# Kernel tuning notes

Measured on AMD Instinct MI355X. Metric: run time of the kernel, lower is better.

Reference implementation:

```python
import jax, jax.numpy as jnp
import numpy as np

DIM = 512
NUM_HEADS = 8
HEAD_DIM = DIM // NUM_HEADS
GAMMA = 1.0


def setup_inputs() -> dict:
    key = jax.random.key(0)
    ks = jax.random.split(key, 10)
    B, S = 2, 2048
    x_real = jax.random.normal(ks[0], (B, S, DIM), dtype=jnp.float32)
    x_imag = jax.random.normal(ks[1], (B, S, DIM), dtype=jnp.float32)
    def xavier(k, fan_in, fan_out):
        lim = float(np.sqrt(6.0 / (fan_in + fan_out)))
        return jax.random.uniform(k, (fan_in, fan_out), jnp.float32, -lim, lim)
    # torch Linear(in,out): weight [out,in]; we store transposed [in,out]
    Wq = xavier(ks[2], 2 * DIM, DIM); bq = jnp.zeros((DIM,), jnp.float32)
    Wk = xavier(ks[3], 2 * DIM, DIM); bk = jnp.zeros((DIM,), jnp.float32)
    Wv = xavier(ks[4], 2 * DIM, DIM); bv = jnp.zeros((DIM,), jnp.float32)
    Wo = xavier(ks[5], DIM, 2 * DIM); bo = jnp.zeros((2 * DIM,), jnp.float32)
    return {"x_real": x_real, "x_imag": x_imag, "Wq": Wq, "bq": bq,
            "Wk": Wk, "bk": bk, "Wv": Wv, "bv": bv, "Wo": Wo, "bo": bo}


def reference(x_real, x_imag, Wq, bq, Wk, bk, Wv, bv, Wo, bo):
    B, S, _ = x_real.shape
    real_embed = jnp.concatenate([x_real, x_imag], axis=-1)  # [B,S,2*dim]
    def proj(W, b):
        y = real_embed @ W + b                               # [B,S,dim]
        return y.reshape(B, S, NUM_HEADS, HEAD_DIM).transpose(0, 2, 1, 3)  # [B,H,S,d]
    Q = proj(Wq, bq)
    K = proj(Wk, bk)
    V = proj(Wv, bv)
    # softmax over head_dim is broadcast-invariant, so the Bhattacharyya
    # coefficient sum_d sqrt(p_i[d]*q_j[d]) factorizes into a matmul.
    sp = jnp.sqrt(jax.nn.softmax(Q, axis=-1))  # [B,H,S,d]
    sq = jnp.sqrt(jax.nn.softmax(K, axis=-1))  # [B,H,S,d]
    bc = jnp.einsum('bhid,bhjd->bhij', sp, sq)  # Bhattacharyya coeff [B,H,S,S]
    bc = jnp.clip(bc, -1.0, 1.0)
    dist = jnp.arccos(bc)
    attn = jax.nn.softmax(-GAMMA * dist * dist, axis=-1)  # [B,H,S,S]
    attended = jnp.einsum('bhij,bhjd->bhid', attn, V)
    attended = attended.transpose(0, 2, 1, 3).reshape(B, S, DIM)
    out = attended @ Wo + bo  # [B,S,2*dim] = concat(real_out, imag_out)
    return out
```

## Files before the change

### kernel.cpp

```cpp
#include <hip/hip_runtime.h>
#include <math.h>


typedef __attribute__((ext_vector_type(8))) short short8;
typedef __attribute__((ext_vector_type(4))) short bf16x4;
typedef __attribute__((ext_vector_type(4))) float f32x4;
typedef __attribute__((ext_vector_type(2))) float f32x2;

#define MFMA(a, b, c) __builtin_amdgcn_mfma_f32_16x16x32_bf16((a), (b), (c), 0, 0, 0)

static __device__ __forceinline__ short f2bf(float f) {
    unsigned u = __float_as_uint(f);
    u += 0x7fffu + ((u >> 16) & 1u);
    return (short)(u >> 16);
}

static __device__ __forceinline__ void gld_lds16(const short* g, short* l) {
    __builtin_amdgcn_global_load_lds(
        (const __attribute__((address_space(1))) unsigned int*)g,
        (__attribute__((address_space(3))) unsigned int*)l, 16, 0, 0);
}

__global__ __launch_bounds__(256) void convert_x(
    const float* __restrict__ xr, const float* __restrict__ xi,
    short* __restrict__ xb)
{
    int idx = blockIdx.x * 256 + threadIdx.x;
    int e = idx << 2;
    int m = e >> 10, k = e & 1023;
    const float* src = (k < 512) ? xr : xi;
    float4 t = *(const float4*)(src + (size_t)m * 512 + (k & 511));
    unsigned lo = (unsigned short)f2bf(t.x) | ((unsigned)(unsigned short)f2bf(t.y) << 16);
    unsigned hi = (unsigned short)f2bf(t.z) | ((unsigned)(unsigned short)f2bf(t.w) << 16);
    uint2 o; o.x = lo; o.y = hi;
    *(uint2*)(xb + e) = o;
}

__global__ __launch_bounds__(256) void transpose_w(
    const float* __restrict__ Wq, const float* __restrict__ Wk,
    const float* __restrict__ Wv, const float* __restrict__ Wo,
    short* __restrict__ wqt, short* __restrict__ wkt,
    short* __restrict__ wvt, short* __restrict__ wot)
{
    __shared__ float t[32][33];
    const int z = blockIdx.z;
    const float* src = (z == 0) ? Wq : (z == 1) ? Wk : (z == 2) ? Wv : Wo;
    short* dst = (z == 0) ? wqt : (z == 1) ? wkt : (z == 2) ? wvt : wot;
    const int K = (z < 3) ? 1024 : 512;
    const int N = (z < 3) ? 512 : 1024;
    const int n0 = blockIdx.x << 5, k0 = blockIdx.y << 5;
    if (n0 >= N || k0 >= K) return;
    const int tx = threadIdx.x & 31, ty = threadIdx.x >> 5;
    #pragma unroll
    for (int i = 0; i < 4; ++i)
        t[ty + 8 * i][tx] = src[(size_t)(k0 + ty + 8 * i) * N + n0 + tx];
    __syncthreads();
    #pragma unroll
    for (int i = 0; i < 4; ++i)
        dst[(size_t)(n0 + ty + 8 * i) * K + k0 + tx] = f2bf(t[tx][ty + 8 * i]);
}

__global__ __launch_bounds__(128, 4) void qkv_mfma(
    const short* __restrict__ xb, const short* __restrict__ wcat,
    const float* __restrict__ bq, const float* __restrict__ bk,
    const float* __restrict__ bv,
    short* __restrict__ sp, short* __restrict__ sq, short* __restrict__ vt)
{
    __shared__ short As[3][128 * 32];
    __shared__ short Bs[3][64 * 32];
    const int jb = blockIdx.x;
    const int m0 = blockIdx.y << 7;
    const int tid = threadIdx.x;
    const int w = tid >> 6, lane = tid & 63;
    const int l = lane & 15, quad = lane >> 4;

    const int srow = lane >> 2;
    const int sseg = (lane & 3) << 3;
    const short* gA = xb   + (size_t)(m0        + (w << 6) + srow) * 1024 + sseg;
    const short* gB = wcat + (size_t)((jb << 6) + (w << 5) + srow) * 1024 + sseg;

    auto STAGE = [&](int bb, int kk) {
        const int k0 = kk << 5;
        #pragma unroll
        for (int t = 0; t < 4; ++t)
            gld_lds16(gA + k0 + t * 16 * 1024, &As[bb][((w << 2) + t) << 9]);
        #pragma unroll
        for (int t = 0; t < 2; ++t)
            gld_lds16(gB + k0 + t * 16 * 1024, &Bs[bb][((w << 1) + t) << 9]);
    };

    STAGE(0, 0);
    STAGE(1, 1);
    asm volatile("s_waitcnt vmcnt(6)" ::: "memory");
    __builtin_amdgcn_s_barrier();

    const f32x4 z4 = {0.f, 0.f, 0.f, 0.f};
    f32x4 acc[4][4];
    #pragma unroll
    for (int i = 0; i < 4; ++i)
        #pragma unroll
        for (int j = 0; j < 4; ++j) acc[i][j] = z4;

    int cb = 0, sb = 2;
    #pragma unroll 1
    for (int kt = 0; kt < 32; ++kt) {
        STAGE(sb, (kt + 2) & 31);
        const short* Al = &As[cb][(w << 6) << 5];
        const short* Bl = &Bs[cb][0];
        short8 af[4], bfr[4];
        #pragma unroll
        for (int i = 0; i < 4; ++i)
            af[i] = *(const short8*)(Al + (((i << 4) + l) << 5) + (quad << 3));
        #pragma unroll
        for (int j = 0; j < 4; ++j)
            bfr[j] = *(const short8*)(Bl + (((j << 4) + l) << 5) + (quad << 3));
        #pragma unroll
        for (int i = 0; i < 4; ++i)
            #pragma unroll
            for (int j = 0; j < 4; ++j)
                acc[i][j] = MFMA(af[i], bfr[j], acc[i][j]);
        asm volatile("s_waitcnt vmcnt(6)" ::: "memory");
        __builtin_amdgcn_s_barrier();
        cb = (cb == 2) ? 0 : cb + 1;
        sb = (sb == 2) ? 0 : sb + 1;
    }
    asm volatile("s_waitcnt vmcnt(0)" ::: "memory");

    const int op = jb >> 3;
    const int h  = jb & 7;

    if (op < 2) {
        short* dst = (op == 0) ? sp : sq;
        const float* bias = (op == 0) ? bq : bk;
        float bcol[4];
        #pragma unroll
        for (int nt = 0; nt < 4; ++nt) bcol[nt] = bias[(h << 6) + (nt << 4) + l];
        #pragma unroll
        for (int i = 0; i < 4; ++i) {
            #pragma unroll
            for (int reg = 0; reg < 4; ++reg) {
                const int r = m0 + (w << 6) + (i << 4) + (quad << 2) + reg;
                const int b = r >> 11, s = r & 2047;
                float v[4];
                #pragma unroll
                for (int nt = 0; nt < 4; ++nt) v[nt] = acc[i][nt][reg] + bcol[nt];
                float mx = fmaxf(fmaxf(v[0], v[1]), fmaxf(v[2], v[3]));
                #pragma unroll
                for (int msk = 1; msk < 16; msk <<= 1) mx = fmaxf(mx, __shfl_xor(mx, msk));
                float e[4], ssum = 0.f;
                #pragma unroll
                for (int nt = 0; nt < 4; ++nt) { e[nt] = __expf(v[nt] - mx); ssum += e[nt]; }
                #pragma unroll
                for (int msk = 1; msk < 16; msk <<= 1) ssum += __shfl_xor(ssum, msk);
                float inv = 1.0f / ssum;
                short* o = dst + ((size_t)((b << 3) + h) * 2048 + s) * 64 + l;
                #pragma unroll
                for (int nt = 0; nt < 4; ++nt)
                    o[nt << 4] = f2bf(sqrtf(e[nt] * inv));
            }
        }
    } else {
        float bcol[4];
        #pragma unroll
        for (int nt = 0; nt < 4; ++nt) bcol[nt] = bv[(h << 6) + (nt << 4) + l];
        #pragma unroll
        for (int i = 0; i < 4; ++i) {
            const int sb2 = m0 + (w << 6) + (i << 4) + (quad << 2);
            const int b = sb2 >> 11, s = sb2 & 2047;
            #pragma unroll
            for (int nt = 0; nt < 4; ++nt) {
                const int d = (nt << 4) + l;
                bf16x4 pk;
                #pragma unroll
                for (int reg = 0; reg < 4; ++reg)
                    pk[reg] = f2bf(acc[i][nt][reg] + bcol[nt]);
                *(bf16x4*)(vt + ((size_t)((b << 3) + h) * 64 + d) * 2048 + s) = pk;
            }
        }
    }
}

__global__ __launch_bounds__(256, 4) void attn_mfma(
    const short* __restrict__ sp, const short* __restrict__ sq,
    const short* __restrict__ vt, short* __restrict__ attB)
{
    __shared__ __align__(16) short sqT[2][64 * 64];
    __shared__ __align__(16) short vtT[2][64 * 64];
    __shared__ __align__(16) short Pb[4][16 * 64];
    __shared__ float denB[4][16];
    const int bh = blockIdx.y;
    const int m0 = blockIdx.x << 6;
    const int tid = threadIdx.x;
    const int w = tid >> 6, lane = tid & 63;
    const int l = lane & 15, quad = lane >> 4;
    const int l7 = l & 7;

    const short* spB = sp + (size_t)bh * 2048 * 64;
    const short* sqB = sq + (size_t)bh * 2048 * 64;
    const short* vtB = vt + (size_t)bh * 64 * 2048;

    const short* apr = spB + (size_t)(m0 + w * 16 + l) * 64 + quad * 8;
    short8 aq0 = *(const short8*)(apr);
    short8 aq1 = *(const short8*)(apr + 32);
    short8 nq0 = aq0 ^ (short)0x8000;
    short8 nq1 = aq1 ^ (short)0x8000;

    const int srow = tid >> 2;
    const int scol = (tid & 3) * 16;
    const short* sqG = sqB + (size_t)srow * 64 + scol;
    const short* vtG = vtB + (size_t)srow * 2048 + scol;
    const int sl0 = (tid & 3) << 1;
    const int sw0 = srow * 64 + (((sl0    ) ^ (srow & 7)) << 3);
    const int sw1 = srow * 64 + (((sl0 | 1) ^ (srow & 7)) << 3);

    const int sRd = (quad ^ l7) << 3;

    {
        short8 a0 = *(const short8*)(sqG);
        short8 a1 = *(const short8*)(sqG + 8);
        short8 b0 = *(const short8*)(vtG);
        short8 b1 = *(const short8*)(vtG + 8);
        *(short8*)(&sqT[0][sw0]) = a0;
        *(short8*)(&sqT[0][sw1]) = a1;
        *(short8*)(&vtT[0][sw0]) = b0;
        *(short8*)(&vtT[0][sw1]) = b1;
    }
    __syncthreads();

    const f32x4 z4 = {0.f, 0.f, 0.f, 0.f};
    const f32x4 ones4 = {1.f, 1.f, 1.f, 1.f};
    f32x4 acc[4] = {z4, z4, z4, z4};
    f32x2 den2 = {0.f, 0.f};
    short* Pw = &Pb[w][0];

    #pragma unroll 1
    for (int jt = 0; jt < 32; ++jt) {
        const int cb = jt & 1, nb = cb ^ 1;
        const int j0n = ((jt + 1) & 31) << 6;
        short8 na0 = *(const short8*)(sqG + (size_t)j0n * 64);
        short8 na1 = *(const short8*)(sqG + (size_t)j0n * 64 + 8);
        short8 nb0 = *(const short8*)(vtG + j0n);
        short8 nb1 = *(const short8*)(vtG + j0n + 8);

        const short* sqL = &sqT[cb][0];
        #pragma unroll
        for (int nt = 0; nt < 4; ++nt) {
            const short* ar = sqL + ((nt * 16 + l) << 6);
            short8 sa0 = *(const short8*)(ar + sRd);
            short8 sa1 = *(const short8*)(ar + (sRd ^ 32));
            f32x4 p = MFMA(sa0, nq0, ones4);
            p = MFMA(sa1, nq1, p);
            f32x2 u01 = {p[0], p[1]};
            f32x2 u23 = {p[2], p[3]};
            const f32x2 zz = {0.f, 0.f};
#if __has_builtin(__builtin_elementwise_max)
            u01 = __builtin_elementwise_max(u01, zz);
            u23 = __builtin_elementwise_max(u23, zz);
#else
            u01.x = fmaxf(u01.x, 0.f); u01.y = fmaxf(u01.y, 0.f);
            u23.x = fmaxf(u23.x, 0.f); u23.y = fmaxf(u23.y, 0.f);
#endif
            f32x2 t01 = {0.000922f, 0.000922f};
            f32x2 t23 = t01;
            t01 = t01 * u01 + 0.00152228f;  t23 = t23 * u23 + 0.00152228f;
            t01 = t01 * u01 + 0.00384801f;  t23 = t23 * u23 + 0.00384801f;
            t01 = t01 * u01 + 0.01015873f;  t23 = t23 * u23 + 0.01015873f;
            t01 = t01 * u01 + 0.02857143f;  t23 = t23 * u23 + 0.02857143f;
            t01 = t01 * u01 + 0.08888889f;  t23 = t23 * u23 + 0.08888889f;
            t01 = t01 * u01 + 0.33333333f;  t23 = t23 * u23 + 0.33333333f;
            t01 = t01 * u01 + 2.0f;         t23 = t23 * u23 + 2.0f;
            f32x2 w01 = u01 * t01;
            f32x2 w23 = u23 * t23;
            float e0 = __expf(-w01.x), e1 = __expf(-w01.y);
            float e2 = __expf(-w23.x), e3 = __expf(-w23.y);
            f32x2 es = {e0 + e2, e1 + e3};
            den2 += es;
            uint2 pk;
            pk.x = (__float_as_uint(e0) >> 16) | (__float_as_uint(e1) & 0xffff0000u);
            pk.y = (__float_as_uint(e2) >> 16) | (__float_as_uint(e3) & 0xffff0000u);
            *(uint2*)(&Pw[(l << 6) + ((((nt << 1) + (quad >> 1)) ^ l7) << 3)
                          + ((quad & 1) << 2)]) = pk;
        }

        const short* pr = Pw + (l << 6);
        short8 pa0 = *(const short8*)(pr + sRd);
        short8 pa1 = *(const short8*)(pr + (sRd ^ 32));
        const short* vL = &vtT[cb][0];
        #pragma unroll
        for (int t4 = 0; t4 < 4; ++t4) {
            const short* vr = vL + ((t4 * 16 + l) << 6);
            short8 vb0 = *(const short8*)(vr + sRd);
            short8 vb1 = *(const short8*)(vr + (sRd ^ 32));
            acc[t4] = MFMA(pa0, vb0, acc[t4]);
            acc[t4] = MFMA(pa1, vb1, acc[t4]);
        }

        *(short8*)(&sqT[nb][sw0]) = na0;
        *(short8*)(&sqT[nb][sw1]) = na1;
        *(short8*)(&vtT[nb][sw0]) = nb0;
        *(short8*)(&vtT[nb][sw1]) = nb1;
        __syncthreads();
    }

    float den = den2.x + den2.y;
    den += __shfl_xor(den, 16);
    den += __shfl_xor(den, 32);
    if (lane < 16) denB[w][l] = den;
    float invd[4];
    #pragma unroll
    for (int reg = 0; reg < 4; ++reg)
        invd[reg] = 1.0f / denB[w][quad * 4 + reg];

    const int b = bh >> 3, hh = bh & 7;
    #pragma unroll
    for (int t4 = 0; t4 < 4; ++t4)
        #pragma unroll
        for (int reg = 0; reg < 4; ++reg) {
            const int row = m0 + w * 16 + quad * 4 + reg;
            attB[((size_t)(b * 2048 + row)) * 512 + hh * 64 + t4 * 16 + l] =
                f2bf(acc[t4][reg] * invd[reg]);
        }
}

__global__ __launch_bounds__(256, 3) void out_mfma(
    const short* __restrict__ attB, const short* __restrict__ wot,
    const float* __restrict__ bo, float* __restrict__ out)
{
    __shared__ short As[3][128 * 32];
    __shared__ short Bs[3][64 * 32];
    const int nb0 = blockIdx.x << 6;
    const int m0 = blockIdx.y << 7;
    const int tid = threadIdx.x;
    const int w = tid >> 6, lane = tid & 63;
    const int l = lane & 15, quad = lane >> 4;

    const short* gA = attB + (size_t)(m0  + (w << 4) + (lane >> 2)) * 512 + ((lane & 3) << 3);
    const short* gB = wot  + (size_t)(nb0 + (w << 4) + (lane >> 2)) * 512 + ((lane & 3) << 3);

    auto STAGE = [&](int bb, int kk) {
        const int k0 = kk << 5;
        gld_lds16(gA + k0,            &As[bb][w << 9]);
        gld_lds16(gA + k0 + 64 * 512, &As[bb][(w + 4) << 9]);
        gld_lds16(gB + k0,            &Bs[bb][w << 9]);
    };

    STAGE(0, 0);
    STAGE(1, 1);
    asm volatile("s_waitcnt vmcnt(3)" ::: "memory");
    __builtin_amdgcn_s_barrier();

    const f32x4 z4 = {0.f, 0.f, 0.f, 0.f};
    f32x4 acc[4][2];
    #pragma unroll
    for (int i = 0; i < 4; ++i) { acc[i][0] = z4; acc[i][1] = z4; }

    const int rsel = (w >> 1) << 6;
    const int csel = (w & 1) << 5;

    int cb = 0, sb = 2;
    #pragma unroll 1
    for (int kt = 0; kt < 16; ++kt) {
        STAGE(sb, (kt + 2) & 15);
        const short* Al = &As[cb][rsel << 5];
        const short* Bl = &Bs[cb][csel << 5];
        short8 af[4], bfr[2];
        #pragma unroll
        for (int i = 0; i < 4; ++i)
            af[i] = *(const short8*)(Al + (((i << 4) + l) << 5) + (quad << 3));
        #pragma unroll
        for (int j = 0; j < 2; ++j)
            bfr[j] = *(const short8*)(Bl + (((j << 4) + l) << 5) + (quad << 3));
        #pragma unroll
        for (int i = 0; i < 4; ++i) {
            acc[i][0] = MFMA(af[i], bfr[0], acc[i][0]);
            acc[i][1] = MFMA(af[i], bfr[1], acc[i][1]);
        }
        asm volatile("s_waitcnt vmcnt(3)" ::: "memory");
        __builtin_amdgcn_s_barrier();
        cb = (cb == 2) ? 0 : cb + 1;
        sb = (sb == 2) ? 0 : sb + 1;
    }
    asm volatile("s_waitcnt vmcnt(0)" ::: "memory");

    const int n0 = nb0 + csel;
    float bcol[2];
    bcol[0] = bo[n0 + l];
    bcol[1] = bo[n0 + 16 + l];
    #pragma unroll
    for (int i = 0; i < 4; ++i)
        #pragma unroll
        for (int reg = 0; reg < 4; ++reg) {
            const int m = m0 + rsel + (i << 4) + (quad << 2) + reg;
            float* o = out + (size_t)m * 1024 + n0 + l;
            o[0]  = acc[i][0][reg] + bcol[0];
            o[16] = acc[i][1][reg] + bcol[1];
        }
}

extern "C" void kernel_launch(void* const* d_in, const int* in_sizes, int n_in,
                              void* d_out, int out_size, void* d_ws, size_t ws_size,
                              hipStream_t stream) {
    const float* xr = (const float*)d_in[0];
    const float* xi = (const float*)d_in[1];
    const float* Wq = (const float*)d_in[2];
    const float* bq = (const float*)d_in[3];
    const float* Wk = (const float*)d_in[4];
    const float* bk = (const float*)d_in[5];
    const float* Wv = (const float*)d_in[6];
    const float* bv = (const float*)d_in[7];
    const float* Wo = (const float*)d_in[8];
    const float* bo = (const float*)d_in[9];
    float* out = (float*)d_out;

    short* base = (short*)d_ws;
    short* xb   = base;
    short* wqt  = xb  + 4194304;
    short* wkt  = wqt + 524288;
    short* wvt  = wkt + 524288;
    short* wot  = wvt + 524288;
    short* spW  = wot + 524288;
    short* sqW  = spW + 2097152;
    short* vtW  = sqW + 2097152;
    short* attB = vtW + 2097152;

    hipLaunchKernelGGL(convert_x, dim3(4096), dim3(256), 0, stream, xr, xi, xb);
    hipLaunchKernelGGL(transpose_w, dim3(32, 32, 4), dim3(256), 0, stream,
                       Wq, Wk, Wv, Wo, wqt, wkt, wvt, wot);
    hipLaunchKernelGGL(qkv_mfma, dim3(24, 32), dim3(128), 0, stream,
                       xb, wqt, bq, bk, bv, spW, sqW, vtW);
    hipLaunchKernelGGL(attn_mfma, dim3(32, 16), dim3(256), 0, stream,
                       spW, sqW, vtW, attB);
    hipLaunchKernelGGL(out_mfma, dim3(16, 32), dim3(256), 0, stream,
                       attB, wot, bo, out);
}
```

Baseline: 185.5 us.

## Use single-wave 64x64 tiles for QKV and output GEMMs, dropping barriers

Both projection GEMMs become one-wavefront-per-block kernels computing 64x64 output tiles. Because a single wave now owns its LDS staging, the workgroup barriers go away and only vmcnt waits remain. The launch grids are doubled to keep the same work, giving more, smaller blocks across the CUs. The cost is no cross-wave sharing of staged tiles, so global loads per FLOP rise for the output GEMM, and latency hiding now depends on occupancy across blocks.

```diff
diff --git a/kernel.cpp b/kernel.cpp
--- a/kernel.cpp
+++ b/kernel.cpp
@@ -60,39 +60,36 @@
         dst[(size_t)(n0 + ty + 8 * i) * K + k0 + tx] = f2bf(t[tx][ty + 8 * i]);
 }
 
-__global__ __launch_bounds__(128, 4) void qkv_mfma(
+__global__ __launch_bounds__(64) void qkv_mfma(
     const short* __restrict__ xb, const short* __restrict__ wcat,
     const float* __restrict__ bq, const float* __restrict__ bk,
     const float* __restrict__ bv,
     short* __restrict__ sp, short* __restrict__ sq, short* __restrict__ vt)
 {
-    __shared__ short As[3][128 * 32];
+    __shared__ short As[3][64 * 32];
     __shared__ short Bs[3][64 * 32];
     const int jb = blockIdx.x;
-    const int m0 = blockIdx.y << 7;
-    const int tid = threadIdx.x;
-    const int w = tid >> 6, lane = tid & 63;
+    const int m0 = blockIdx.y << 6;
+    const int lane = threadIdx.x;
     const int l = lane & 15, quad = lane >> 4;
 
     const int srow = lane >> 2;
     const int sseg = (lane & 3) << 3;
-    const short* gA = xb   + (size_t)(m0        + (w << 6) + srow) * 1024 + sseg;
-    const short* gB = wcat + (size_t)((jb << 6) + (w << 5) + srow) * 1024 + sseg;
+    const short* gA = xb   + (size_t)(m0        + srow) * 1024 + sseg;
+    const short* gB = wcat + (size_t)((jb << 6) + srow) * 1024 + sseg;
 
     auto STAGE = [&](int bb, int kk) {
         const int k0 = kk << 5;
         #pragma unroll
-        for (int t = 0; t < 4; ++t)
-            gld_lds16(gA + k0 + t * 16 * 1024, &As[bb][((w << 2) + t) << 9]);
-        #pragma unroll
-        for (int t = 0; t < 2; ++t)
-            gld_lds16(gB + k0 + t * 16 * 1024, &Bs[bb][((w << 1) + t) << 9]);
+        for (int t = 0; t < 4; ++t) {
+            gld_lds16(gA + k0 + t * 16 * 1024, &As[bb][t << 9]);
+            gld_lds16(gB + k0 + t * 16 * 1024, &Bs[bb][t << 9]);
+        }
     };
 
     STAGE(0, 0);
     STAGE(1, 1);
-    asm volatile("s_waitcnt vmcnt(6)" ::: "memory");
-    __builtin_amdgcn_s_barrier();
+    asm volatile("s_waitcnt vmcnt(8)" ::: "memory");
 
     const f32x4 z4 = {0.f, 0.f, 0.f, 0.f};
     f32x4 acc[4][4];
@@ -105,7 +102,7 @@
     #pragma unroll 1
     for (int kt = 0; kt < 32; ++kt) {
         STAGE(sb, (kt + 2) & 31);
-        const short* Al = &As[cb][(w << 6) << 5];
+        const short* Al = &As[cb][0];
         const short* Bl = &Bs[cb][0];
         short8 af[4], bfr[4];
         #pragma unroll
@@ -119,12 +116,10 @@
             #pragma unroll
             for (int j = 0; j < 4; ++j)
                 acc[i][j] = MFMA(af[i], bfr[j], acc[i][j]);
-        asm volatile("s_waitcnt vmcnt(6)" ::: "memory");
-        __builtin_amdgcn_s_barrier();
+        asm volatile("s_waitcnt vmcnt(8)" ::: "memory");
         cb = (cb == 2) ? 0 : cb + 1;
         sb = (sb == 2) ? 0 : sb + 1;
     }
-    asm volatile("s_waitcnt vmcnt(0)" ::: "memory");
 
     const int op = jb >> 3;
     const int h  = jb & 7;
@@ -139,7 +134,7 @@
         for (int i = 0; i < 4; ++i) {
             #pragma unroll
             for (int reg = 0; reg < 4; ++reg) {
-                const int r = m0 + (w << 6) + (i << 4) + (quad << 2) + reg;
+                const int r = m0 + (i << 4) + (quad << 2) + reg;
                 const int b = r >> 11, s = r & 2047;
                 float v[4];
                 #pragma unroll
@@ -165,7 +160,7 @@
         for (int nt = 0; nt < 4; ++nt) bcol[nt] = bv[(h << 6) + (nt << 4) + l];
         #pragma unroll
         for (int i = 0; i < 4; ++i) {
-            const int sb2 = m0 + (w << 6) + (i << 4) + (quad << 2);
+            const int sb2 = m0 + (i << 4) + (quad << 2);
             const int b = sb2 >> 11, s = sb2 & 2047;
             #pragma unroll
             for (int nt = 0; nt < 4; ++nt) {
@@ -322,78 +317,77 @@
         }
 }
 
-__global__ __launch_bounds__(256, 3) void out_mfma(
+__global__ __launch_bounds__(64) void out_mfma(
     const short* __restrict__ attB, const short* __restrict__ wot,
     const float* __restrict__ bo, float* __restrict__ out)
 {
-    __shared__ short As[3][128 * 32];
+    __shared__ short As[3][64 * 32];
     __shared__ short Bs[3][64 * 32];
-    const int nb0 = blockIdx.x << 6;
-    const int m0 = blockIdx.y << 7;
-    const int tid = threadIdx.x;
-    const int w = tid >> 6, lane = tid & 63;
+    const int n0 = blockIdx.x << 6;
+    const int m0 = blockIdx.y << 6;
+    const int lane = threadIdx.x;
     const int l = lane & 15, quad = lane >> 4;
 
-    const short* gA = attB + (size_t)(m0  + (w << 4) + (lane >> 2)) * 512 + ((lane & 3) << 3);
-    const short* gB = wot  + (size_t)(nb0 + (w << 4) + (lane >> 2)) * 512 + ((lane & 3) << 3);
+    const int srow = lane >> 2;
+    const int sseg = (lane & 3) << 3;
+    const short* gA = attB + (size_t)(m0 + srow) * 512 + sseg;
+    const short* gB = wot  + (size_t)(n0 + srow) * 512 + sseg;
 
     auto STAGE = [&](int bb, int kk) {
         const int k0 = kk << 5;
-        gld_lds16(gA + k0,            &As[bb][w << 9]);
-        gld_lds16(gA + k0 + 64 * 512, &As[bb][(w + 4) << 9]);
-        gld_lds16(gB + k0,            &Bs[bb][w << 9]);
+        #pragma unroll
+        for (int t = 0; t < 4; ++t) {
+            gld_lds16(gA + k0 + t * 16 * 512, &As[bb][t << 9]);
+            gld_lds16(gB + k0 + t * 16 * 512, &Bs[bb][t << 9]);
+        }
     };
 
     STAGE(0, 0);
     STAGE(1, 1);
-    asm volatile("s_waitcnt vmcnt(3)" ::: "memory");
-    __builtin_amdgcn_s_barrier();
+    asm volatile("s_waitcnt vmcnt(8)" ::: "memory");
 
     const f32x4 z4 = {0.f, 0.f, 0.f, 0.f};
-    f32x4 acc[4][2];
-    #pragma unroll
-    for (int i = 0; i < 4; ++i) { acc[i][0] = z4; acc[i][1] = z4; }
-
-    const int rsel = (w >> 1) << 6;
-    const int csel = (w & 1) << 5;
+    f32x4 acc[4][4];
+    #pragma unroll
+    for (int i = 0; i < 4; ++i)
+        #pragma unroll
+        for (int j = 0; j < 4; ++j) acc[i][j] = z4;
 
     int cb = 0, sb = 2;
     #pragma unroll 1
     for (int kt = 0; kt < 16; ++kt) {
         STAGE(sb, (kt + 2) & 15);
-        const short* Al = &As[cb][rsel << 5];
-        const short* Bl = &Bs[cb][csel << 5];
-        short8 af[4], bfr[2];
+        const short* Al = &As[cb][0];
+        const short* Bl = &Bs[cb][0];
+        short8 af[4], bfr[4];
         #pragma unroll
         for (int i = 0; i < 4; ++i)
             af[i] = *(const short8*)(Al + (((i << 4) + l) << 5) + (quad << 3));
         #pragma unroll
-        for (int j = 0; j < 2; ++j)
+        for (int j = 0; j < 4; ++j)
             bfr[j] = *(const short8*)(Bl + (((j << 4) + l) << 5) + (quad << 3));
         #pragma unroll
-        for (int i = 0; i < 4; ++i) {
-            acc[i][0] = MFMA(af[i], bfr[0], acc[i][0]);
-            acc[i][1] = MFMA(af[i], bfr[1], acc[i][1]);
-        }
-        asm volatile("s_waitcnt vmcnt(3)" ::: "memory");
-        __builtin_amdgcn_s_barrier();
+        for (int i = 0; i < 4; ++i)
+            #pragma unroll
+            for (int j = 0; j < 4; ++j)
+                acc[i][j] = MFMA(af[i], bfr[j], acc[i][j]);
+        asm volatile("s_waitcnt vmcnt(8)" ::: "memory");
         cb = (cb == 2) ? 0 : cb + 1;
         sb = (sb == 2) ? 0 : sb + 1;
     }
-    asm volatile("s_waitcnt vmcnt(0)" ::: "memory");
-
-    const int n0 = nb0 + csel;
-    float bcol[2];
-    bcol[0] = bo[n0 + l];
-    bcol[1] = bo[n0 + 16 + l];
+
+    float bcol[4];
+    #pragma unroll
+    for (int nt = 0; nt < 4; ++nt) bcol[nt] = bo[n0 + (nt << 4) + l];
     #pragma unroll
     for (int i = 0; i < 4; ++i)
         #pragma unroll
         for (int reg = 0; reg < 4; ++reg) {
-            const int m = m0 + rsel + (i << 4) + (quad << 2) + reg;
+            const int m = m0 + (i << 4) + (quad << 2) + reg;
             float* o = out + (size_t)m * 1024 + n0 + l;
-            o[0]  = acc[i][0][reg] + bcol[0];
-            o[16] = acc[i][1][reg] + bcol[1];
+            #pragma unroll
+            for (int nt = 0; nt < 4; ++nt)
+                o[nt << 4] = acc[i][nt][reg] + bcol[nt];
         }
 }
 
@@ -426,10 +420,10 @@
     hipLaunchKernelGGL(convert_x, dim3(4096), dim3(256), 0, stream, xr, xi, xb);
     hipLaunchKernelGGL(transpose_w, dim3(32, 32, 4), dim3(256), 0, stream,
                        Wq, Wk, Wv, Wo, wqt, wkt, wvt, wot);
-    hipLaunchKernelGGL(qkv_mfma, dim3(24, 32), dim3(128), 0, stream,
+    hipLaunchKernelGGL(qkv_mfma, dim3(24, 64), dim3(64), 0, stream,
                        xb, wqt, bq, bk, bv, spW, sqW, vtW);
     hipLaunchKernelGGL(attn_mfma, dim3(32, 16), dim3(256), 0, stream,
                        spW, sqW, vtW, attB);
-    hipLaunchKernelGGL(out_mfma, dim3(16, 32), dim3(256), 0, stream,
+    hipLaunchKernelGGL(out_mfma, dim3(16, 64), dim3(64), 0, stream,
                        attB, wot, bo, out);
 }
```

Measured after the change: 184.6 us. About the same (-0.5%).
